# Optimization experiments

Measured on AMD Instinct MI355X. Metric: run time of the kernel, lower is better.

Reference implementation:

```python
import jax, jax.numpy as jnp
import numpy as np

B, T, D = 2, 2048, 4096
H, KH, HD = 32, 8, 128          # n_heads, n_kv_heads, head_dim = D // H
WINDOW, NGLOBAL = 1024, 32      # sliding window size, global sink tokens
ROPE_BASE = 500000.0


def _rope_tables(seq_len, dim):
    inv_freq = 1.0 / (ROPE_BASE ** (np.arange(0, dim, 2, dtype=np.float64) / dim))
    freqs = np.outer(np.arange(seq_len, dtype=np.float64), inv_freq)
    emb = np.concatenate([freqs, freqs], axis=-1)  # [T, HD]
    cos = jnp.asarray(np.cos(emb), dtype=jnp.float32)[None, None]  # [1,1,T,HD]
    sin = jnp.asarray(np.sin(emb), dtype=jnp.float32)[None, None]
    return cos, sin


def _window_global_mask(seq_len, window, n_global):
    i = np.arange(seq_len)[:, None]  # query pos
    j = np.arange(seq_len)[None, :]  # key pos
    causal = j <= i
    local = j > (i - window)
    global_keys = j < n_global
    return jnp.asarray(causal & (local | global_keys))[None, None]  # [1,1,T,T] bool


def rotate_half(x):
    x1, x2 = jnp.split(x, 2, axis=-1)
    return jnp.concatenate([-x2, x1], axis=-1)


def setup_inputs() -> dict:
    key = jax.random.key(0)
    kx, kq, kk, kv, ko = jax.random.split(key, 5)
    s = 1.0 / np.sqrt(D)
    x = jax.random.normal(kx, (B, T, D), dtype=jnp.float32)
    # Linear weights stored [in, out] (y = x @ W), same math as torch's x @ W.T
    Wq = jax.random.normal(kq, (D, H * HD), dtype=jnp.float32) * s
    Wk = jax.random.normal(kk, (D, KH * HD), dtype=jnp.float32) * s
    Wv = jax.random.normal(kv, (D, KH * HD), dtype=jnp.float32) * s
    Wo = jax.random.normal(ko, (H * HD, D), dtype=jnp.float32) * s
    cos, sin = _rope_tables(T, HD)
    mask = _window_global_mask(T, WINDOW, NGLOBAL)
    return {"x": x, "Wq": Wq, "Wk": Wk, "Wv": Wv, "Wo": Wo,
            "cos": cos, "sin": sin, "mask": mask}


def reference(x, Wq, Wk, Wv, Wo, cos, sin, mask):
    Bx, Tx, Dx = x.shape
    q = (x @ Wq).reshape(Bx, Tx, H, HD).transpose(0, 2, 1, 3)   # [B,H,T,HD]
    k = (x @ Wk).reshape(Bx, Tx, KH, HD).transpose(0, 2, 1, 3)  # [B,KH,T,HD]
    v = (x @ Wv).reshape(Bx, Tx, KH, HD).transpose(0, 2, 1, 3)
    # RoPE
    q = q * cos + rotate_half(q) * sin
    k = k * cos + rotate_half(k) * sin
    # GQA: repeat_interleave KV heads to match query heads (faithful to source)
    factor = H // KH
    k = jnp.repeat(k, factor, axis=1)  # [B,H,T,HD]
    v = jnp.repeat(v, factor, axis=1)
    # SDPA with dense bool mask (True = attend), default scale 1/sqrt(HD)
    scale = 1.0 / np.sqrt(HD)
    scores = jnp.einsum('bhqd,bhkd->bhqk', q, k) * scale  # [B,H,T,T]
    scores = jnp.where(mask, scores, jnp.finfo(scores.dtype).min)
    attn = jax.nn.softmax(scores, axis=-1)
    out = jnp.einsum('bhqk,bhkd->bhqd', attn, v)
    out = out.transpose(0, 2, 1, 3).reshape(Bx, Tx, H * HD)
    return out @ Wo
```

## Files before the change

### kernel.cpp

```cpp
#include <hip/hip_runtime.h>
#include <stdint.h>

typedef unsigned short u16;
typedef __bf16 bf16x8 __attribute__((ext_vector_type(8)));
typedef float f32x4 __attribute__((ext_vector_type(4)));

#define D_MODEL 4096
#define T_SEQ   2048
#define B_SZ    2
#define NH      32
#define NKV     8
#define HDIM    128
#define WINDOW  1024
#define NGLOB   32
#define QSTR    6144

static constexpr float SCALE = 0.08838834764831845f;

__device__ __forceinline__ u16 f2b(float f) {
  __bf16 h = (__bf16)f;
  return __builtin_bit_cast(u16, h);
}

__global__ __launch_bounds__(256) void convert_bf16_kernel(const float* __restrict__ in,
                                                           u16* __restrict__ outp, int n4) {
  int i = blockIdx.x * 256 + threadIdx.x;
  if (i >= n4) return;
  float4 v = ((const float4*)in)[i];
  ushort4 o;
  o.x = f2b(v.x); o.y = f2b(v.y); o.z = f2b(v.z); o.w = f2b(v.w);
  ((ushort4*)outp)[i] = o;
}

__global__ __launch_bounds__(256) void transpose_w_kernel(const float* __restrict__ W,
                                                          u16* __restrict__ Wt, int Kd, int Nd) {
  __shared__ float tile[32][33];
  int tx = threadIdx.x & 31, ty = threadIdx.x >> 5;
  int bx = blockIdx.x * 32;
  int by = blockIdx.y * 32;
#pragma unroll
  for (int i = 0; i < 4; ++i)
    tile[ty + i * 8][tx] = W[(size_t)(by + ty + i * 8) * Nd + bx + tx];
  __syncthreads();
#pragma unroll
  for (int i = 0; i < 4; ++i)
    Wt[(size_t)(bx + ty + i * 8) * Kd + by + tx] = f2b(tile[tx][ty + i * 8]);
}

__global__ __launch_bounds__(256) void transpose_v_kernel(const u16* __restrict__ in,
                                                          u16* __restrict__ outp) {
  __shared__ u16 tile[32][33];
  int tx = threadIdx.x & 31, ty = threadIdx.x >> 5;
  int x0 = blockIdx.x * 32;
  int t0 = blockIdx.y * 32;
  int b = blockIdx.z;
  const u16* src = in + (size_t)b * T_SEQ * QSTR;
  u16* dst = outp + (size_t)b * (NKV * HDIM) * T_SEQ;
#pragma unroll
  for (int i = 0; i < 4; ++i)
    tile[ty + i * 8][tx] = src[(size_t)(t0 + ty + i * 8) * QSTR + x0 + tx];
  __syncthreads();
#pragma unroll
  for (int i = 0; i < 4; ++i)
    dst[(size_t)(x0 + ty + i * 8) * T_SEQ + t0 + tx] = tile[tx][ty + i * 8];
}

template <typename CT>
__global__ __launch_bounds__(512, 2) void gemm256_kernel(const u16* __restrict__ A,
                                                         const u16* __restrict__ Bt,
                                                         CT* __restrict__ C,
                                                         int ldc, int K) {
  __shared__ u16 sh[65536];
  const int tid = threadIdx.x;
  const int wave = tid >> 6, lane = tid & 63;
  const int g = lane >> 4, li = lane & 15;
  const int wr = wave >> 2, wc = wave & 3;
  const int m0 = blockIdx.y * 256, n0 = blockIdx.x * 256;
  const int r0 = tid >> 3;
  const int cs = ((tid & 7) ^ ((tid >> 3) & 7)) << 3;
  const u16* pA = A + (size_t)(m0 + r0) * K + cs;
  const u16* pB = Bt + (size_t)(n0 + r0) * K + cs;
  const int sl0 = (g ^ (li & 7)) << 3;
  const int sl1 = ((4 + g) ^ (li & 7)) << 3;
  const int nT = K >> 6;

  f32x4 acc[8][4];
  f32x4 zz = {0.f, 0.f, 0.f, 0.f};
#pragma unroll
  for (int M = 0; M < 8; ++M)
#pragma unroll
    for (int n = 0; n < 4; ++n) acc[M][n] = zz;

  auto stage = [&](const u16* src0, int ts, int dstBase) {
#pragma unroll
    for (int i = 0; i < 2; ++i) {
      const u16* s = src0 + (size_t)(i * 64) * K + ts * 64;
      __builtin_amdgcn_global_load_lds((__attribute__((address_space(1))) void*)s,
                                       (__attribute__((address_space(3))) void*)(sh + dstBase + i * 4096 + wave * 512),
                                       16, 0, 0);
    }
  };

  stage(pA, 0, 0);
  stage(pA + (size_t)128 * K, 0, 8192);
  stage(pB, 0, 16384);
  stage(pB + (size_t)128 * K, 0, 24576);
  stage(pB, 1, 32768 + 16384);
  stage(pB + (size_t)128 * K, 1, 32768 + 24576);
  stage(pA, 1, 32768);
  asm volatile("s_waitcnt vmcnt(6)" ::: "memory");
  __builtin_amdgcn_s_barrier();

  bf16x8 afr[4][2], bfr[4][2];
  for (int t = 0; t < nT; ++t) {
    const int cur = t & 1;
    const int ab = cur * 32768, bb = ab + 16384;
    const int nb = (cur ^ 1) * 32768;
    const int tn1 = (t + 1 < nT) ? t + 1 : nT - 1;
    const int tn2 = (t + 2 < nT) ? t + 2 : nT - 1;
#pragma unroll
    for (int n = 0; n < 4; ++n) {
      int row = wc * 64 + n * 16 + li;
      bfr[n][0] = *(const bf16x8*)&sh[bb + row * 64 + sl0];
      bfr[n][1] = *(const bf16x8*)&sh[bb + row * 64 + sl1];
    }
#pragma unroll
    for (int m = 0; m < 4; ++m) {
      int row = wr * 128 + m * 16 + li;
      afr[m][0] = *(const bf16x8*)&sh[ab + row * 64 + sl0];
      afr[m][1] = *(const bf16x8*)&sh[ab + row * 64 + sl1];
    }
    stage(pA + (size_t)128 * K, tn1, nb + 8192);
    __builtin_amdgcn_s_barrier();
    asm volatile("s_waitcnt lgkmcnt(0)" ::: "memory");
    __builtin_amdgcn_sched_barrier(0);
    __builtin_amdgcn_s_setprio(1);
#pragma unroll
    for (int m = 0; m < 4; ++m)
#pragma unroll
      for (int n = 0; n < 2; ++n) {
        acc[m][n] = __builtin_amdgcn_mfma_f32_16x16x32_bf16(afr[m][0], bfr[n][0], acc[m][n], 0, 0, 0);
        acc[m][n] = __builtin_amdgcn_mfma_f32_16x16x32_bf16(afr[m][1], bfr[n][1], acc[m][n], 0, 0, 0);
      }
    __builtin_amdgcn_s_setprio(0);
    __builtin_amdgcn_s_barrier();
    stage(pB, tn2, bb);
    __builtin_amdgcn_s_barrier();
    __builtin_amdgcn_s_setprio(1);
#pragma unroll
    for (int m = 0; m < 4; ++m)
#pragma unroll
      for (int n = 2; n < 4; ++n) {
        acc[m][n] = __builtin_amdgcn_mfma_f32_16x16x32_bf16(afr[m][0], bfr[n][0], acc[m][n], 0, 0, 0);
        acc[m][n] = __builtin_amdgcn_mfma_f32_16x16x32_bf16(afr[m][1], bfr[n][1], acc[m][n], 0, 0, 0);
      }
    __builtin_amdgcn_s_setprio(0);
    __builtin_amdgcn_s_barrier();
#pragma unroll
    for (int m = 0; m < 4; ++m) {
      int row = wr * 128 + 64 + m * 16 + li;
      afr[m][0] = *(const bf16x8*)&sh[ab + row * 64 + sl0];
      afr[m][1] = *(const bf16x8*)&sh[ab + row * 64 + sl1];
    }
    stage(pB + (size_t)128 * K, tn2, bb + 8192);
    __builtin_amdgcn_s_barrier();
    asm volatile("s_waitcnt lgkmcnt(0)" ::: "memory");
    __builtin_amdgcn_sched_barrier(0);
    __builtin_amdgcn_s_setprio(1);
#pragma unroll
    for (int m = 0; m < 4; ++m)
#pragma unroll
      for (int n = 0; n < 2; ++n) {
        acc[4 + m][n] = __builtin_amdgcn_mfma_f32_16x16x32_bf16(afr[m][0], bfr[n][0], acc[4 + m][n], 0, 0, 0);
        acc[4 + m][n] = __builtin_amdgcn_mfma_f32_16x16x32_bf16(afr[m][1], bfr[n][1], acc[4 + m][n], 0, 0, 0);
      }
    __builtin_amdgcn_s_setprio(0);
    __builtin_amdgcn_s_barrier();
    stage(pA, tn2, ab);
    __builtin_amdgcn_s_barrier();
    __builtin_amdgcn_s_setprio(1);
#pragma unroll
    for (int m = 0; m < 4; ++m)
#pragma unroll
      for (int n = 2; n < 4; ++n) {
        acc[4 + m][n] = __builtin_amdgcn_mfma_f32_16x16x32_bf16(afr[m][0], bfr[n][0], acc[4 + m][n], 0, 0, 0);
        acc[4 + m][n] = __builtin_amdgcn_mfma_f32_16x16x32_bf16(afr[m][1], bfr[n][1], acc[4 + m][n], 0, 0, 0);
      }
    __builtin_amdgcn_s_setprio(0);
    asm volatile("s_waitcnt vmcnt(6)" ::: "memory");
    __builtin_amdgcn_s_barrier();
  }
#pragma unroll
  for (int M = 0; M < 8; ++M)
#pragma unroll
    for (int n = 0; n < 4; ++n)
#pragma unroll
      for (int r = 0; r < 4; ++r) {
        int row = m0 + wr * 128 + M * 16 + g * 4 + r;
        int col = n0 + wc * 64 + n * 16 + li;
        if constexpr (sizeof(CT) == 2)
          C[(size_t)row * ldc + col] = (CT)f2b(acc[M][n][r]);
        else
          C[(size_t)row * ldc + col] = acc[M][n][r];
      }
}

__global__ __launch_bounds__(512, 2) void gemm192_kernel(const u16* __restrict__ A,
                                                         const u16* __restrict__ Bt,
                                                         u16* __restrict__ C,
                                                         int ldc, int K) {
  __shared__ u16 sh[57344];
  const int tid = threadIdx.x;
  const int wave = tid >> 6, lane = tid & 63;
  const int g = lane >> 4, li = lane & 15;
  const int wr = wave >> 2, wc = wave & 3;
  const int m0 = blockIdx.y * 256, n0 = blockIdx.x * 192;
  const int r0 = tid >> 3;
  const int cs = ((tid & 7) ^ ((tid >> 3) & 7)) << 3;
  const u16* pA = A + (size_t)(m0 + r0) * K + cs;
  const u16* pB = Bt + (size_t)(n0 + r0) * K + cs;
  const int sl0 = (g ^ (li & 7)) << 3;
  const int sl1 = ((4 + g) ^ (li & 7)) << 3;
  const int nT = K >> 6;

  f32x4 acc[8][3];
  f32x4 zz = {0.f, 0.f, 0.f, 0.f};
#pragma unroll
  for (int M = 0; M < 8; ++M)
#pragma unroll
    for (int n = 0; n < 3; ++n) acc[M][n] = zz;

  auto stage64 = [&](const u16* src0, int ts, int dstU16) {
    __builtin_amdgcn_global_load_lds(
        (__attribute__((address_space(1))) void*)(src0 + (size_t)ts * 64),
        (__attribute__((address_space(3))) void*)(sh + dstU16 + wave * 512), 16, 0, 0);
  };

#pragma unroll
  for (int u = 0; u < 4; ++u) stage64(pA + (size_t)(u * 64) * K, 0, u * 4096);
#pragma unroll
  for (int u = 0; u < 3; ++u) stage64(pB + (size_t)(u * 64) * K, 0, 16384 + u * 4096);
#pragma unroll
  for (int u = 0; u < 4; ++u) stage64(pA + (size_t)(u * 64) * K, 1, 28672 + u * 4096);
#pragma unroll
  for (int u = 0; u < 3; ++u) stage64(pB + (size_t)(u * 64) * K, 1, 28672 + 16384 + u * 4096);
  asm volatile("s_waitcnt vmcnt(7)" ::: "memory");
  __builtin_amdgcn_s_barrier();

  bf16x8 afr[4][2], bfr[3][2];
  for (int t = 0; t < nT; ++t) {
    const int ab = (t & 1) * 28672, bb = ab + 16384;
    const int tn2 = (t + 2 < nT) ? t + 2 : nT - 1;
#pragma unroll
    for (int n = 0; n < 3; ++n) {
      int row = wc * 48 + n * 16 + li;
      bfr[n][0] = *(const bf16x8*)&sh[bb + row * 64 + sl0];
      bfr[n][1] = *(const bf16x8*)&sh[bb + row * 64 + sl1];
    }
#pragma unroll
    for (int m = 0; m < 4; ++m) {
      int row = wr * 128 + m * 16 + li;
      afr[m][0] = *(const bf16x8*)&sh[ab + row * 64 + sl0];
      afr[m][1] = *(const bf16x8*)&sh[ab + row * 64 + sl1];
    }
    __builtin_amdgcn_s_barrier();
    asm volatile("s_waitcnt lgkmcnt(0)" ::: "memory");
    __builtin_amdgcn_sched_barrier(0);
    __builtin_amdgcn_s_setprio(1);
#pragma unroll
    for (int m = 0; m < 4; ++m)
#pragma unroll
      for (int n = 0; n < 2; ++n) {
        acc[m][n] = __builtin_amdgcn_mfma_f32_16x16x32_bf16(afr[m][0], bfr[n][0], acc[m][n], 0, 0, 0);
        acc[m][n] = __builtin_amdgcn_mfma_f32_16x16x32_bf16(afr[m][1], bfr[n][1], acc[m][n], 0, 0, 0);
      }
    __builtin_amdgcn_s_setprio(0);
    __builtin_amdgcn_s_barrier();
    stage64(pB, tn2, bb);
    stage64(pB + (size_t)64 * K, tn2, bb + 4096);
    stage64(pA, tn2, ab);
    __builtin_amdgcn_s_barrier();
    __builtin_amdgcn_s_setprio(1);
#pragma unroll
    for (int m = 0; m < 4; ++m) {
      acc[m][2] = __builtin_amdgcn_mfma_f32_16x16x32_bf16(afr[m][0], bfr[2][0], acc[m][2], 0, 0, 0);
      acc[m][2] = __builtin_amdgcn_mfma_f32_16x16x32_bf16(afr[m][1], bfr[2][1], acc[m][2], 0, 0, 0);
    }
    __builtin_amdgcn_s_setprio(0);
    __builtin_amdgcn_s_barrier();
#pragma unroll
    for (int m = 0; m < 4; ++m) {
      int row = wr * 128 + 64 + m * 16 + li;
      afr[m][0] = *(const bf16x8*)&sh[ab + row * 64 + sl0];
      afr[m][1] = *(const bf16x8*)&sh[ab + row * 64 + sl1];
    }
    stage64(pB + (size_t)128 * K, tn2, bb + 8192);
    stage64(pA + (size_t)128 * K, tn2, ab + 8192);
    __builtin_amdgcn_s_barrier();
    asm volatile("s_waitcnt lgkmcnt(0)" ::: "memory");
    __builtin_amdgcn_sched_barrier(0);
    __builtin_amdgcn_s_setprio(1);
#pragma unroll
    for (int m = 0; m < 4; ++m)
#pragma unroll
      for (int n = 0; n < 2; ++n) {
        acc[4 + m][n] = __builtin_amdgcn_mfma_f32_16x16x32_bf16(afr[m][0], bfr[n][0], acc[4 + m][n], 0, 0, 0);
        acc[4 + m][n] = __builtin_amdgcn_mfma_f32_16x16x32_bf16(afr[m][1], bfr[n][1], acc[4 + m][n], 0, 0, 0);
      }
    __builtin_amdgcn_s_setprio(0);
    __builtin_amdgcn_s_barrier();
    stage64(pA + (size_t)64 * K, tn2, ab + 4096);
    stage64(pA + (size_t)192 * K, tn2, ab + 12288);
    __builtin_amdgcn_s_barrier();
    __builtin_amdgcn_s_setprio(1);
#pragma unroll
    for (int m = 0; m < 4; ++m) {
      acc[4 + m][2] = __builtin_amdgcn_mfma_f32_16x16x32_bf16(afr[m][0], bfr[2][0], acc[4 + m][2], 0, 0, 0);
      acc[4 + m][2] = __builtin_amdgcn_mfma_f32_16x16x32_bf16(afr[m][1], bfr[2][1], acc[4 + m][2], 0, 0, 0);
    }
    __builtin_amdgcn_s_setprio(0);
    asm volatile("s_waitcnt vmcnt(7)" ::: "memory");
    __builtin_amdgcn_s_barrier();
  }
#pragma unroll
  for (int M = 0; M < 8; ++M)
#pragma unroll
    for (int n = 0; n < 3; ++n)
#pragma unroll
      for (int r = 0; r < 4; ++r) {
        int row = m0 + wr * 128 + M * 16 + g * 4 + r;
        int col = n0 + wc * 48 + n * 16 + li;
        C[(size_t)row * ldc + col] = f2b(acc[M][n][r]);
      }
}

__global__ __launch_bounds__(256) void rope_kernel(u16* __restrict__ qkv,
                                                   const float* __restrict__ cosp,
                                                   const float* __restrict__ sinp) {
  int idx = blockIdx.x * 256 + threadIdx.x;
  int d8 = idx & 7;
  int rest = idx >> 3;
  int hh = rest % (NH + NKV);
  int bt = rest / (NH + NKV);
  if (bt >= B_SZ * T_SEQ) return;
  int tok = bt & (T_SEQ - 1);
  int d0 = d8 * 8;
  const float4* cp = (const float4*)(cosp + (size_t)tok * HDIM + d0);
  const float4* sp = (const float4*)(sinp + (size_t)tok * HDIM + d0);
  float4 cA = cp[0], cB = cp[1];
  float4 sA = sp[0], sB = sp[1];
  float cc[8] = {cA.x, cA.y, cA.z, cA.w, cB.x, cB.y, cB.z, cB.w};
  float ss[8] = {sA.x, sA.y, sA.z, sA.w, sB.x, sB.y, sB.z, sB.w};
  float scl = (hh < NH) ? SCALE : 1.0f;
  u16* base = qkv + (size_t)bt * QSTR + hh * HDIM;
  bf16x8 v1 = *(const bf16x8*)(base + d0);
  bf16x8 v2 = *(const bf16x8*)(base + d0 + 64);
  bf16x8 o1, o2;
#pragma unroll
  for (int j = 0; j < 8; ++j) {
    float xa = (float)v1[j], xb = (float)v2[j];
    o1[j] = (__bf16)((xa * cc[j] - xb * ss[j]) * scl);
    o2[j] = (__bf16)((xb * cc[j] + xa * ss[j]) * scl);
  }
  *(bf16x8*)(base + d0) = o1;
  *(bf16x8*)(base + d0 + 64) = o2;
}

__global__ __launch_bounds__(512) void attn_kernel(const u16* __restrict__ qp,
                                                   const u16* __restrict__ kp,
                                                   const u16* __restrict__ vtp,
                                                   u16* __restrict__ ctx) {
  __shared__ u16 Kt[2][64 * 128];
  __shared__ u16 Vt[2][128 * 64];
  __shared__ u16 Pl[8][16 * 64];
  int tid = threadIdx.x;
  int w = tid >> 6, lane = tid & 63;
  int g = lane >> 4, li = lane & 15;
  int i0 = blockIdx.x * 128;
  int h = blockIdx.y, b = blockIdx.z;
  int kh = h >> 2;
  f32x4 zz = {0.f, 0.f, 0.f, 0.f};

  bf16x8 qf[4];
  size_t qrow = (size_t)(b * T_SEQ + i0 + w * 16 + li) * QSTR + h * HDIM;
#pragma unroll
  for (int c = 0; c < 4; ++c) qf[c] = *(const bf16x8*)(qp + qrow + c * 32 + g * 8);

  f32x4 o[8];
#pragma unroll
  for (int f = 0; f < 8; ++f) o[f] = zz;
  float m_s = -1e30f, l_s = 0.f;
  const int irow = i0 + w * 16 + li;

  const int jlo = (i0 > WINDOW) ? (i0 - WINDOW) : 0;
  const int nglob = (jlo > 0) ? 1 : 0;
  const int ntiles = nglob + (i0 + 64 - jlo) / 64 + 1;

  auto j_of = [&](int t) { return (nglob && t == 0) ? 0 : jlo + (t - nglob) * 64; };

  auto stage = [&](int t, int buf) {
    int j0 = j_of(t);
#pragma unroll
    for (int i = 0; i < 2; ++i) {
      int o8 = tid + 512 * i;
      int krow = o8 >> 4, kch = o8 & 15;
      size_t gk = (size_t)(b * T_SEQ + j0 + krow) * QSTR + kh * HDIM + (kch ^ (krow & 7)) * 8;
      __builtin_amdgcn_global_load_lds((__attribute__((address_space(1))) void*)(kp + gk),
                                       (__attribute__((address_space(3))) void*)(Kt[buf] + o8 * 8),
                                       16, 0, 0);
      int vrow = o8 >> 3, vch = o8 & 7;
      size_t gv = ((size_t)(b * NKV + kh) * HDIM + vrow) * T_SEQ + j0 + (vch ^ (vrow & 7)) * 8;
      __builtin_amdgcn_global_load_lds((__attribute__((address_space(1))) void*)(vtp + gv),
                                       (__attribute__((address_space(3))) void*)(Vt[buf] + o8 * 8),
                                       16, 0, 0);
    }
  };

  stage(0, 0);
  asm volatile("s_waitcnt vmcnt(0)" ::: "memory");
  __builtin_amdgcn_s_barrier();

  for (int t = 0; t < ntiles; ++t) {
    const int buf = t & 1;
    const int j0 = j_of(t);
    if (t + 1 < ntiles) stage(t + 1, buf ^ 1);

    f32x4 s[4];
#pragma unroll
    for (int kb = 0; kb < 4; ++kb) s[kb] = zz;
#pragma unroll
    for (int c = 0; c < 4; ++c) {
      int hd0 = c * 32 + g * 8;
#pragma unroll
      for (int kb = 0; kb < 4; ++kb) {
        int key = kb * 16 + li;
        bf16x8 kf = *(const bf16x8*)&Kt[buf][(key * 128 + hd0) ^ ((key & 7) << 3)];
        s[kb] = __builtin_amdgcn_mfma_f32_16x16x32_bf16(kf, qf[c], s[kb], 0, 0, 0);
      }
    }

    float x[4][4];
    float mt = -1e30f;
#pragma unroll
    for (int kb = 0; kb < 4; ++kb)
#pragma unroll
      for (int r = 0; r < 4; ++r) {
        int j = j0 + kb * 16 + g * 4 + r;
        bool vm = (j <= irow) && ((j > irow - WINDOW) || (j < NGLOB));
        float xx = vm ? s[kb][r] : -1e30f;
        x[kb][r] = xx;
        mt = fmaxf(mt, xx);
      }
    mt = fmaxf(mt, __shfl_xor(mt, 16, 64));
    mt = fmaxf(mt, __shfl_xor(mt, 32, 64));
    float mn = fmaxf(m_s, mt);
    float corr = __expf(m_s - mn);
    m_s = mn;
    float rs = 0.f;
#pragma unroll
    for (int kb = 0; kb < 4; ++kb) {
      ushort4 pk;
#pragma unroll
      for (int r = 0; r < 4; ++r) {
        float p = __expf(x[kb][r] - mn);
        rs += p;
        ((u16*)&pk)[r] = f2b(p);
      }
      *(ushort4*)&Pl[w][(li * 64 + kb * 16 + g * 4) ^ ((li & 7) << 3)] = pk;
    }
    rs += __shfl_xor(rs, 16, 64);
    rs += __shfl_xor(rs, 32, 64);
    l_s = l_s * corr + rs;

    float c4[4];
#pragma unroll
    for (int r = 0; r < 4; ++r) c4[r] = __shfl(corr, g * 4 + r, 16);
#pragma unroll
    for (int f = 0; f < 8; ++f) {
      o[f][0] *= c4[0]; o[f][1] *= c4[1];
      o[f][2] *= c4[2]; o[f][3] *= c4[3];
    }

    bf16x8 pa0 = *(const bf16x8*)&Pl[w][(li * 64 + 0 + g * 8) ^ ((li & 7) << 3)];
    bf16x8 pa1 = *(const bf16x8*)&Pl[w][(li * 64 + 32 + g * 8) ^ ((li & 7) << 3)];

#pragma unroll
    for (int f = 0; f < 8; ++f) {
      int hd = f * 16 + li;
      bf16x8 v0 = *(const bf16x8*)&Vt[buf][(hd * 64 + 0 + g * 8) ^ ((li & 7) << 3)];
      bf16x8 v1 = *(const bf16x8*)&Vt[buf][(hd * 64 + 32 + g * 8) ^ ((li & 7) << 3)];
      o[f] = __builtin_amdgcn_mfma_f32_16x16x32_bf16(pa0, v0, o[f], 0, 0, 0);
      o[f] = __builtin_amdgcn_mfma_f32_16x16x32_bf16(pa1, v1, o[f], 0, 0, 0);
    }

    asm volatile("s_waitcnt vmcnt(0)" ::: "memory");
    __builtin_amdgcn_s_barrier();
  }

  float l4[4];
#pragma unroll
  for (int r = 0; r < 4; ++r) l4[r] = __shfl(l_s, g * 4 + r, 16);
#pragma unroll
  for (int f = 0; f < 8; ++f)
#pragma unroll
    for (int r = 0; r < 4; ++r) {
      size_t orow = (size_t)(b * T_SEQ + i0 + w * 16 + g * 4 + r) * (NH * HDIM) + h * HDIM + f * 16 + li;
      ctx[orow] = f2b(o[f][r] / l4[r]);
    }
}

extern "C" void kernel_launch(void* const* d_in, const int* in_sizes, int n_in,
                              void* d_out, int out_size, void* d_ws, size_t ws_size,
                              hipStream_t stream) {
  const float* x    = (const float*)d_in[0];
  const float* Wq   = (const float*)d_in[1];
  const float* Wk   = (const float*)d_in[2];
  const float* Wv   = (const float*)d_in[3];
  const float* Wo   = (const float*)d_in[4];
  const float* cosp = (const float*)d_in[5];
  const float* sinp = (const float*)d_in[6];

  char* ws = (char*)d_ws;
  u16* xb     = (u16*)(ws + 0ull);
  u16* Wqkvt  = (u16*)(ws + 33554432ull);
  u16* Wot    = (u16*)(ws + 83886080ull);
  u16* qkv    = (u16*)(ws + 117440512ull);
  u16* ctx    = xb;
  u16* vT     = Wqkvt;

  convert_bf16_kernel<<<16384, 256, 0, stream>>>(x, xb, 4194304);
  transpose_w_kernel<<<dim3(128, 128), 256, 0, stream>>>(Wq, Wqkvt, 4096, 4096);
  transpose_w_kernel<<<dim3(32, 128), 256, 0, stream>>>(Wk, Wqkvt + (size_t)4096 * 4096, 4096, 1024);
  transpose_w_kernel<<<dim3(32, 128), 256, 0, stream>>>(Wv, Wqkvt + (size_t)5120 * 4096, 4096, 1024);
  transpose_w_kernel<<<dim3(128, 128), 256, 0, stream>>>(Wo, Wot, 4096, 4096);

  gemm192_kernel<<<dim3(32, 16), 512, 0, stream>>>(xb, Wqkvt, qkv, QSTR, 4096);

  transpose_v_kernel<<<dim3(32, 64, 2), 256, 0, stream>>>(qkv + 5120, vT);

  rope_kernel<<<5120, 256, 0, stream>>>(qkv, cosp, sinp);

  attn_kernel<<<dim3(16, 32, 2), 512, 0, stream>>>(qkv, qkv + 4096, vT, ctx);

  gemm256_kernel<float><<<dim3(16, 16), 512, 0, stream>>>(ctx, Wot, (float*)d_out, 4096, 4096);
}
```

Baseline: 558.1 us.

## Process two 16-row query groups per wave to reuse staged K/V tiles

Each attention block now covers 256 query rows instead of 128. Each wave handles two 16-row query groups that share the same K and V fragments read from LDS. This halves the grid and the global/LDS traffic for K and V per query row, and lets the QK and PV MFMAs interleave across two independent accumulators. The cost is roughly double the accumulator registers, which may lower occupancy, plus a few extra masked tiles per block from the wider query span, with only 512 blocks to spread over the GPU.

```diff
diff --git a/kernel.cpp b/kernel.cpp
--- a/kernel.cpp
+++ b/kernel.cpp
@@ -376,25 +376,29 @@
   int tid = threadIdx.x;
   int w = tid >> 6, lane = tid & 63;
   int g = lane >> 4, li = lane & 15;
-  int i0 = blockIdx.x * 128;
+  int i0 = blockIdx.x * 256;
   int h = blockIdx.y, b = blockIdx.z;
   int kh = h >> 2;
   f32x4 zz = {0.f, 0.f, 0.f, 0.f};
 
-  bf16x8 qf[4];
-  size_t qrow = (size_t)(b * T_SEQ + i0 + w * 16 + li) * QSTR + h * HDIM;
-#pragma unroll
-  for (int c = 0; c < 4; ++c) qf[c] = *(const bf16x8*)(qp + qrow + c * 32 + g * 8);
-
-  f32x4 o[8];
-#pragma unroll
-  for (int f = 0; f < 8; ++f) o[f] = zz;
-  float m_s = -1e30f, l_s = 0.f;
-  const int irow = i0 + w * 16 + li;
+  bf16x8 qf0[4], qf1[4];
+  size_t qr0 = (size_t)(b * T_SEQ + i0 + w * 32 + li) * QSTR + h * HDIM;
+  size_t qr1 = qr0 + (size_t)16 * QSTR;
+#pragma unroll
+  for (int c = 0; c < 4; ++c) {
+    qf0[c] = *(const bf16x8*)(qp + qr0 + c * 32 + g * 8);
+    qf1[c] = *(const bf16x8*)(qp + qr1 + c * 32 + g * 8);
+  }
+
+  f32x4 o0[8], o1[8];
+#pragma unroll
+  for (int f = 0; f < 8; ++f) { o0[f] = zz; o1[f] = zz; }
+  float m_s0 = -1e30f, l_s0 = 0.f, m_s1 = -1e30f, l_s1 = 0.f;
+  const int ir0 = i0 + w * 32 + li, ir1 = ir0 + 16;
 
   const int jlo = (i0 > WINDOW) ? (i0 - WINDOW) : 0;
   const int nglob = (jlo > 0) ? 1 : 0;
-  const int ntiles = nglob + (i0 + 64 - jlo) / 64 + 1;
+  const int ntiles = nglob + (i0 + 192 - jlo) / 64 + 1;
 
   auto j_of = [&](int t) { return (nglob && t == 0) ? 0 : jlo + (t - nglob) * 64; };
 
@@ -425,9 +429,9 @@
     const int j0 = j_of(t);
     if (t + 1 < ntiles) stage(t + 1, buf ^ 1);
 
-    f32x4 s[4];
-#pragma unroll
-    for (int kb = 0; kb < 4; ++kb) s[kb] = zz;
+    f32x4 s0[4], s1[4];
+#pragma unroll
+    for (int kb = 0; kb < 4; ++kb) { s0[kb] = zz; s1[kb] = zz; }
 #pragma unroll
     for (int c = 0; c < 4; ++c) {
       int hd0 = c * 32 + g * 8;
@@ -435,77 +439,89 @@
       for (int kb = 0; kb < 4; ++kb) {
         int key = kb * 16 + li;
         bf16x8 kf = *(const bf16x8*)&Kt[buf][(key * 128 + hd0) ^ ((key & 7) << 3)];
-        s[kb] = __builtin_amdgcn_mfma_f32_16x16x32_bf16(kf, qf[c], s[kb], 0, 0, 0);
-      }
-    }
-
-    float x[4][4];
-    float mt = -1e30f;
-#pragma unroll
-    for (int kb = 0; kb < 4; ++kb)
-#pragma unroll
-      for (int r = 0; r < 4; ++r) {
-        int j = j0 + kb * 16 + g * 4 + r;
-        bool vm = (j <= irow) && ((j > irow - WINDOW) || (j < NGLOB));
-        float xx = vm ? s[kb][r] : -1e30f;
-        x[kb][r] = xx;
-        mt = fmaxf(mt, xx);
-      }
-    mt = fmaxf(mt, __shfl_xor(mt, 16, 64));
-    mt = fmaxf(mt, __shfl_xor(mt, 32, 64));
-    float mn = fmaxf(m_s, mt);
-    float corr = __expf(m_s - mn);
-    m_s = mn;
-    float rs = 0.f;
-#pragma unroll
-    for (int kb = 0; kb < 4; ++kb) {
-      ushort4 pk;
-#pragma unroll
-      for (int r = 0; r < 4; ++r) {
-        float p = __expf(x[kb][r] - mn);
-        rs += p;
-        ((u16*)&pk)[r] = f2b(p);
-      }
-      *(ushort4*)&Pl[w][(li * 64 + kb * 16 + g * 4) ^ ((li & 7) << 3)] = pk;
-    }
-    rs += __shfl_xor(rs, 16, 64);
-    rs += __shfl_xor(rs, 32, 64);
-    l_s = l_s * corr + rs;
-
-    float c4[4];
-#pragma unroll
-    for (int r = 0; r < 4; ++r) c4[r] = __shfl(corr, g * 4 + r, 16);
-#pragma unroll
-    for (int f = 0; f < 8; ++f) {
-      o[f][0] *= c4[0]; o[f][1] *= c4[1];
-      o[f][2] *= c4[2]; o[f][3] *= c4[3];
-    }
-
-    bf16x8 pa0 = *(const bf16x8*)&Pl[w][(li * 64 + 0 + g * 8) ^ ((li & 7) << 3)];
-    bf16x8 pa1 = *(const bf16x8*)&Pl[w][(li * 64 + 32 + g * 8) ^ ((li & 7) << 3)];
+        s0[kb] = __builtin_amdgcn_mfma_f32_16x16x32_bf16(kf, qf0[c], s0[kb], 0, 0, 0);
+        s1[kb] = __builtin_amdgcn_mfma_f32_16x16x32_bf16(kf, qf1[c], s1[kb], 0, 0, 0);
+      }
+    }
+
+    bf16x8 pa00, pa01, pa10, pa11;
+    auto softmax_p = [&](f32x4* s, int irow, float& m_s, float& l_s,
+                         bf16x8& paA, bf16x8& paB, f32x4* o) {
+      float x[4][4];
+      float mt = -1e30f;
+#pragma unroll
+      for (int kb = 0; kb < 4; ++kb)
+#pragma unroll
+        for (int r = 0; r < 4; ++r) {
+          int j = j0 + kb * 16 + g * 4 + r;
+          bool vm = (j <= irow) && ((j > irow - WINDOW) || (j < NGLOB));
+          float xx = vm ? s[kb][r] : -1e30f;
+          x[kb][r] = xx;
+          mt = fmaxf(mt, xx);
+        }
+      mt = fmaxf(mt, __shfl_xor(mt, 16, 64));
+      mt = fmaxf(mt, __shfl_xor(mt, 32, 64));
+      float mn = fmaxf(m_s, mt);
+      float corr = __expf(m_s - mn);
+      m_s = mn;
+      float rs = 0.f;
+#pragma unroll
+      for (int kb = 0; kb < 4; ++kb) {
+        ushort4 pk;
+#pragma unroll
+        for (int r = 0; r < 4; ++r) {
+          float p = __expf(x[kb][r] - mn);
+          rs += p;
+          ((u16*)&pk)[r] = f2b(p);
+        }
+        *(ushort4*)&Pl[w][(li * 64 + kb * 16 + g * 4) ^ ((li & 7) << 3)] = pk;
+      }
+      rs += __shfl_xor(rs, 16, 64);
+      rs += __shfl_xor(rs, 32, 64);
+      l_s = l_s * corr + rs;
+      float c4[4];
+#pragma unroll
+      for (int r = 0; r < 4; ++r) c4[r] = __shfl(corr, g * 4 + r, 16);
+#pragma unroll
+      for (int f = 0; f < 8; ++f) {
+        o[f][0] *= c4[0]; o[f][1] *= c4[1];
+        o[f][2] *= c4[2]; o[f][3] *= c4[3];
+      }
+      paA = *(const bf16x8*)&Pl[w][(li * 64 + 0 + g * 8) ^ ((li & 7) << 3)];
+      paB = *(const bf16x8*)&Pl[w][(li * 64 + 32 + g * 8) ^ ((li & 7) << 3)];
+    };
+    softmax_p(s0, ir0, m_s0, l_s0, pa00, pa01, o0);
+    softmax_p(s1, ir1, m_s1, l_s1, pa10, pa11, o1);
 
 #pragma unroll
     for (int f = 0; f < 8; ++f) {
       int hd = f * 16 + li;
       bf16x8 v0 = *(const bf16x8*)&Vt[buf][(hd * 64 + 0 + g * 8) ^ ((li & 7) << 3)];
       bf16x8 v1 = *(const bf16x8*)&Vt[buf][(hd * 64 + 32 + g * 8) ^ ((li & 7) << 3)];
-      o[f] = __builtin_amdgcn_mfma_f32_16x16x32_bf16(pa0, v0, o[f], 0, 0, 0);
-      o[f] = __builtin_amdgcn_mfma_f32_16x16x32_bf16(pa1, v1, o[f], 0, 0, 0);
+      o0[f] = __builtin_amdgcn_mfma_f32_16x16x32_bf16(pa00, v0, o0[f], 0, 0, 0);
+      o0[f] = __builtin_amdgcn_mfma_f32_16x16x32_bf16(pa01, v1, o0[f], 0, 0, 0);
+      o1[f] = __builtin_amdgcn_mfma_f32_16x16x32_bf16(pa10, v0, o1[f], 0, 0, 0);
+      o1[f] = __builtin_amdgcn_mfma_f32_16x16x32_bf16(pa11, v1, o1[f], 0, 0, 0);
     }
 
     asm volatile("s_waitcnt vmcnt(0)" ::: "memory");
     __builtin_amdgcn_s_barrier();
   }
 
-  float l4[4];
-#pragma unroll
-  for (int r = 0; r < 4; ++r) l4[r] = __shfl(l_s, g * 4 + r, 16);
+  float l40[4], l41[4];
+#pragma unroll
+  for (int r = 0; r < 4; ++r) {
+    l40[r] = __shfl(l_s0, g * 4 + r, 16);
+    l41[r] = __shfl(l_s1, g * 4 + r, 16);
+  }
 #pragma unroll
   for (int f = 0; f < 8; ++f)
 #pragma unroll
     for (int r = 0; r < 4; ++r) {
-      size_t orow = (size_t)(b * T_SEQ + i0 + w * 16 + g * 4 + r) * (NH * HDIM) + h * HDIM + f * 16 + li;
-      ctx[orow] = f2b(o[f][r] / l4[r]);
+      size_t row0 = (size_t)(b * T_SEQ + i0 + w * 32 + g * 4 + r) * (NH * HDIM) + h * HDIM + f * 16 + li;
+      ctx[row0] = f2b(o0[f][r] / l40[r]);
+      size_t row1 = row0 + (size_t)16 * (NH * HDIM);
+      ctx[row1] = f2b(o1[f][r] / l41[r]);
     }
 }
 
@@ -540,7 +556,7 @@
 
   rope_kernel<<<5120, 256, 0, stream>>>(qkv, cosp, sinp);
 
-  attn_kernel<<<dim3(16, 32, 2), 512, 0, stream>>>(qkv, qkv + 4096, vT, ctx);
+  attn_kernel<<<dim3(8, 32, 2), 512, 0, stream>>>(qkv, qkv + 4096, vT, ctx);
 
   gemm256_kernel<float><<<dim3(16, 16), 512, 0, stream>>>(ctx, Wot, (float*)d_out, 4096, 4096);
 }
```

After: 527.8 us, median of 3. 1.06x faster.
